# Performance work log

Measured on AMD Instinct MI355X. Metric: run time of the kernel, lower is better.

## Reference

```python
import jax, jax.numpy as jnp
import numpy as np

D_MODEL = 1024
NUM_HEADS = 16
HEAD_DIM = D_MODEL // NUM_HEADS


def setup_inputs() -> dict:
    key = jax.random.key(0)
    ks = jax.random.split(key, 10)
    B, SQ, SK = 2, 2048, 2048
    scale = 1.0 / np.sqrt(D_MODEL)
    inp = {
        "x1": jax.random.normal(ks[0], (B, SQ, D_MODEL), jnp.float32),
        "x2": jax.random.normal(ks[1], (B, SK, D_MODEL), jnp.float32),
        "Wq": jax.random.normal(ks[2], (D_MODEL, D_MODEL), jnp.float32) * scale,
        "bq": jnp.zeros((D_MODEL,), jnp.float32),
        "Wk": jax.random.normal(ks[3], (D_MODEL, D_MODEL), jnp.float32) * scale,
        "bk": jnp.zeros((D_MODEL,), jnp.float32),
        "Wv": jax.random.normal(ks[4], (D_MODEL, D_MODEL), jnp.float32) * scale,
        "bv": jnp.zeros((D_MODEL,), jnp.float32),
        "Wo": jax.random.normal(ks[5], (D_MODEL, D_MODEL), jnp.float32) * scale,
        "bo": jnp.zeros((D_MODEL,), jnp.float32),
    }
    return inp


def reference(x1, x2, Wq, bq, Wk, bk, Wv, bv, Wo, bo):
    B, SQ, _ = x1.shape
    SK = x2.shape[1]
    # projections, then split into heads: [B, H, S, Dh]
    def split_heads(t, S):
        return t.reshape(B, S, NUM_HEADS, HEAD_DIM).transpose(0, 2, 1, 3)
    Q = split_heads(x1 @ Wq + bq, SQ)
    K = split_heads(x2 @ Wk + bk, SK)
    V = split_heads(x2 @ Wv + bv, SK)
    # note: original scales by 1/head_dim**0.5
    scores = jnp.einsum("bhqd,bhkd->bhqk", Q, K) / jnp.sqrt(
        jnp.asarray(HEAD_DIM, Q.dtype))
    attn = jax.nn.softmax(scores, axis=-1)
    ctx = jnp.einsum("bhqk,bhkd->bhqd", attn, V)
    ctx = ctx.transpose(0, 2, 1, 3).reshape(B, SQ, D_MODEL)
    return ctx @ Wo + bo
```

## Files before the change

### kernel.cpp

```cpp
#include <hip/hip_runtime.h>
#include <stdint.h>


typedef unsigned short u16b;
typedef __attribute__((ext_vector_type(4))) short short4v;
typedef __attribute__((ext_vector_type(8))) short short8v;
typedef __attribute__((ext_vector_type(4))) float float4v;
typedef __attribute__((ext_vector_type(2))) unsigned int uint2v;

#if __has_builtin(__builtin_amdgcn_exp2f)
__device__ __forceinline__ float exp2_fast(float x){ return __builtin_amdgcn_exp2f(x); }
#else
__device__ __forceinline__ float exp2_fast(float x){ return exp2f(x); }
#endif

__device__ __forceinline__ u16b f2bf(float f) {
  union { float f; unsigned int i; } v; v.f = f;
  return (u16b)((v.i + 0x7fffu + ((v.i >> 16) & 1u)) >> 16);
}
__device__ __forceinline__ void gl_lds16(const u16b* g, u16b* l) {
  __builtin_amdgcn_global_load_lds(
      (const __attribute__((address_space(1))) void*)g,
      (__attribute__((address_space(3))) void*)l, 16, 0, 0);
}

#define FENCE_BARRIER() do { asm volatile("" ::: "memory"); \
  __builtin_amdgcn_s_barrier(); asm volatile("" ::: "memory"); } while(0)
#define LGKM0() do { asm volatile("s_waitcnt lgkmcnt(0)" ::: "memory"); \
  __builtin_amdgcn_sched_barrier(0); } while(0)
#define VMCNT(n) do { asm volatile("s_waitcnt vmcnt(" #n ")" ::: "memory"); \
  __builtin_amdgcn_sched_barrier(0); } while(0)

__global__ __launch_bounds__(256) void prep(
    const float* __restrict__ x1, const float* __restrict__ x2,
    const float* __restrict__ W0, const float* __restrict__ W1,
    const float* __restrict__ W2, const float* __restrict__ W3,
    u16b* __restrict__ x1b, u16b* __restrict__ x2b, u16b* __restrict__ WT) {
  const int tid = threadIdx.x;
  const int mode = blockIdx.y;
  if (mode < 2) {
    const float* src = mode ? x2 : x1;
    u16b* dst = mode ? x2b : x1b;
    const int n4 = 1024*1024;
    int i = blockIdx.x * 256 + tid;
    const int stride = gridDim.x * 256;
    for (; i < n4; i += stride) {
      float4v v = ((const float4v*)src)[i];
      short4v o;
      o[0]=(short)f2bf(v[0]); o[1]=(short)f2bf(v[1]);
      o[2]=(short)f2bf(v[2]); o[3]=(short)f2bf(v[3]);
      ((short4v*)dst)[i] = o;
    }
  } else {
    __shared__ u16b tile[32][33];
    const int z = mode - 2;
    const float* src = (z==0) ? W0 : (z==1) ? W1 : (z==2) ? W2 : W3;
    u16b* dst = WT + (size_t)z * (1024*1024);
    const int x = tid & 31, y = tid >> 5;
    const int bx = (blockIdx.x & 31) * 32, by = (blockIdx.x >> 5) * 32;
#pragma unroll
    for (int j=0;j<4;++j)
      tile[y*4+j][x] = f2bf(src[(size_t)(by + y*4+j)*1024 + bx + x]);
    __syncthreads();
#pragma unroll
    for (int j=0;j<4;++j)
      dst[(size_t)(bx + y*4+j)*1024 + by + x] = tile[x][y*4+j];
  }
}

template<bool BIAS_ROW>
__device__ __forceinline__ void gemm256_core(
    u16b* __restrict__ As, u16b* __restrict__ Bs,
    const u16b* __restrict__ A, const u16b* __restrict__ Bt,
    const float* __restrict__ bias, u16b* __restrict__ C,
    int N, int K, int bm, int bn, float oscale) {
  constexpr int ASTR = 256*64, BSTR = 256*64;
  const int tid = threadIdx.x;
  const int lane = tid & 63, wave = tid >> 6;
  const int wr = wave >> 2, wc = wave & 3;
  const int l15 = lane & 15, l4 = lane >> 4;

  auto stage_half = [&](const u16b* __restrict__ G, int row0, int k0,
                        u16b* __restrict__ Lbase) {
#pragma unroll
    for (int j=0;j<2;++j) {
      int idx = j*512 + tid;
      int row = idx >> 3, seg = idx & 7;
      int segg = seg ^ (row & 7);
      gl_lds16(&G[(size_t)(row0+row)*K + k0 + segg*8], &Lbase[idx*8]);
    }
  };

  float4v acc[2][2][4][2];
#pragma unroll
  for (int qm=0;qm<2;++qm)
#pragma unroll
  for (int qn=0;qn<2;++qn)
#pragma unroll
  for (int m=0;m<4;++m)
#pragma unroll
  for (int n=0;n<2;++n) acc[qm][qn][m][n] = (float4v){0.f,0.f,0.f,0.f};

  const int NK = K >> 6;
  stage_half(A,  bm+0,   0,  As + 0);
  stage_half(Bt, bn+0,   0,  Bs + 0);
  stage_half(A,  bm+128, 0,  As + 128*64);
  stage_half(Bt, bn+128, 0,  Bs + 128*64);
  stage_half(A,  bm+0,   64, As + ASTR);
  stage_half(Bt, bn+0,   64, Bs + BSTR);
  VMCNT(4);
  FENCE_BARRIER();

  int cur = 0;
  for (int t = 0; t < NK; ++t) {
    u16b* Ac = As + cur*ASTR;  u16b* Bc = Bs + cur*BSTR;
    u16b* An = As + (cur^1)*ASTR;  u16b* Bn = Bs + (cur^1)*BSTR;
    const int k1 = (t+1) << 6, k2 = (t+2) << 6;
    short8v af[4][2], bf0[2][2], bf1[2][2];

#pragma unroll
    for (int m=0;m<4;++m)
#pragma unroll
      for (int ks=0;ks<2;++ks)
        af[m][ks] = *(const short8v*)&Ac[(0*128 + wr*64 + m*16 + l15)*64
                                         + (((ks*4+l4) ^ (l15&7))*8)];
#pragma unroll
    for (int n=0;n<2;++n)
#pragma unroll
      for (int ks=0;ks<2;++ks)
        bf0[n][ks] = *(const short8v*)&Bc[(0*128 + wc*32 + n*16 + l15)*64
                                          + (((ks*4+l4) ^ (l15&7))*8)];
    if (t+1 < NK) stage_half(A, bm+128, k1, An + 128*64);
    FENCE_BARRIER();
    LGKM0();
    __builtin_amdgcn_s_setprio(1);
#pragma unroll
    for (int m=0;m<4;++m)
#pragma unroll
      for (int n=0;n<2;++n)
#pragma unroll
        for (int ks=0;ks<2;++ks)
          acc[0][0][m][n] = __builtin_amdgcn_mfma_f32_16x16x32_bf16(
              af[m][ks], bf0[n][ks], acc[0][0][m][n], 0, 0, 0);
    __builtin_amdgcn_s_setprio(0);
    FENCE_BARRIER();

#pragma unroll
    for (int n=0;n<2;++n)
#pragma unroll
      for (int ks=0;ks<2;++ks)
        bf1[n][ks] = *(const short8v*)&Bc[(1*128 + wc*32 + n*16 + l15)*64
                                          + (((ks*4+l4) ^ (l15&7))*8)];
    if (t+1 < NK) stage_half(Bt, bn+128, k1, Bn + 128*64);
    FENCE_BARRIER();
    LGKM0();
    __builtin_amdgcn_s_setprio(1);
#pragma unroll
    for (int m=0;m<4;++m)
#pragma unroll
      for (int n=0;n<2;++n)
#pragma unroll
        for (int ks=0;ks<2;++ks)
          acc[0][1][m][n] = __builtin_amdgcn_mfma_f32_16x16x32_bf16(
              af[m][ks], bf1[n][ks], acc[0][1][m][n], 0, 0, 0);
    __builtin_amdgcn_s_setprio(0);
    FENCE_BARRIER();

#pragma unroll
    for (int m=0;m<4;++m)
#pragma unroll
      for (int ks=0;ks<2;++ks)
        af[m][ks] = *(const short8v*)&Ac[(1*128 + wr*64 + m*16 + l15)*64
                                         + (((ks*4+l4) ^ (l15&7))*8)];
    if (t+2 < NK) stage_half(A, bm+0, k2, Ac + 0);
    FENCE_BARRIER();
    LGKM0();
    __builtin_amdgcn_s_setprio(1);
#pragma unroll
    for (int m=0;m<4;++m)
#pragma unroll
      for (int n=0;n<2;++n)
#pragma unroll
        for (int ks=0;ks<2;++ks)
          acc[1][0][m][n] = __builtin_amdgcn_mfma_f32_16x16x32_bf16(
              af[m][ks], bf0[n][ks], acc[1][0][m][n], 0, 0, 0);
    __builtin_amdgcn_s_setprio(0);
    FENCE_BARRIER();

    if (t+2 < NK) stage_half(Bt, bn+0, k2, Bc + 0);
    FENCE_BARRIER();
    LGKM0();
    __builtin_amdgcn_s_setprio(1);
#pragma unroll
    for (int m=0;m<4;++m)
#pragma unroll
      for (int n=0;n<2;++n)
#pragma unroll
        for (int ks=0;ks<2;++ks)
          acc[1][1][m][n] = __builtin_amdgcn_mfma_f32_16x16x32_bf16(
              af[m][ks], bf1[n][ks], acc[1][1][m][n], 0, 0, 0);
    __builtin_amdgcn_s_setprio(0);
    if (t == NK-2) { VMCNT(0); }
    else          { VMCNT(4); }
    FENCE_BARRIER();
    cur ^= 1;
  }

#pragma unroll
  for (int qm=0;qm<2;++qm)
#pragma unroll
  for (int qn=0;qn<2;++qn)
#pragma unroll
  for (int n=0;n<2;++n) {
    int col = bn + qn*128 + wc*32 + n*16 + l15;
    float bbc = BIAS_ROW ? 0.f : bias[col];
#pragma unroll
    for (int m=0;m<4;++m) {
      int row0 = bm + qm*128 + wr*64 + m*16 + l4*4;
#pragma unroll
      for (int r=0;r<4;++r) {
        float bb = BIAS_ROW ? bias[row0+r] : bbc;
        float v = (acc[qm][qn][m][n][r] + bb) * oscale;
        C[(size_t)(row0+r)*N + col] = f2bf(v);
      }
    }
  }
}

__global__ __launch_bounds__(512, 2) void gemm_qkv256(
    const u16b* __restrict__ x1b, const u16b* __restrict__ x2b,
    const u16b* __restrict__ WT, const float* __restrict__ bq,
    const float* __restrict__ bk, const float* __restrict__ bv,
    u16b* __restrict__ QKV) {
  __shared__ __align__(16) u16b As[2*256*64];
  __shared__ __align__(16) u16b Bs[2*256*64];
  const int f = blockIdx.x;
  const int z = f >> 6;
  const int u = f & 63;
  const int w = ((u & 7) << 3) | (u >> 3);
  const size_t Mi = 1024*1024;
  const float QSCALE = 0.125f * 1.4426950408889634f;
  if (z == 2) {
    int bm = (w >> 4) * 256;
    int bn = (w & 15) * 256;
    gemm256_core<true>(As, Bs, WT + 2*Mi, x2b, bv, QKV + 8*Mi,
                       4096, 1024, bm, bn, 1.0f);
  } else {
    int bm = (w >> 2) * 256;
    int bn = (w & 3) * 256;
    gemm256_core<false>(As, Bs, z ? x2b : x1b, WT + (size_t)z*Mi,
                        z ? bk : bq, QKV + (size_t)z*4*Mi,
                        1024, 1024, bm, bn, z ? 1.0f : QSCALE);
  }
}

template<int BN, bool OUT_F32, bool BIAS_ROW>
__device__ __forceinline__ void gemm_core(
    u16b* __restrict__ As, u16b* __restrict__ Bs,
    const u16b* __restrict__ A, const u16b* __restrict__ Bt,
    const float* __restrict__ bias, void* __restrict__ Cv,
    int N, int K, int bm, int bn, float oscale) {
  constexpr int NT = BN / 32;
  constexpr int ASTRIDE = 128*64;
  constexpr int BSTRIDE = BN*64;
  const int tid = threadIdx.x;
  const int lane = tid & 63, wave = tid >> 6;
  const int wm = wave >> 1, wn = wave & 1;
  const int l15 = lane & 15, l4 = lane >> 4;
  float4v acc[4][NT];
#pragma unroll
  for (int i=0;i<4;++i)
#pragma unroll
    for (int j=0;j<NT;++j) acc[i][j] = (float4v){0.f,0.f,0.f,0.f};

  auto stage = [&](int buf, int k0) {
#pragma unroll
    for (int j=0;j<4;++j) {
      int idx = j*256 + tid;
      int row = idx >> 3, seg = idx & 7;
      int segg = seg ^ (row & 7);
      gl_lds16(&A[(size_t)(bm+row)*K + k0 + segg*8], &As[buf*ASTRIDE + idx*8]);
    }
#pragma unroll
    for (int j=0;j<BN/32;++j) {
      int idx = j*256 + tid;
      int row = idx >> 3, seg = idx & 7;
      int segg = seg ^ (row & 7);
      gl_lds16(&Bt[(size_t)(bn+row)*K + k0 + segg*8], &Bs[buf*BSTRIDE + idx*8]);
    }
  };

  const int NK = K >> 6;
  stage(0, 0);
  __syncthreads();
  for (int kt = 0; kt < NK; ++kt) {
    const int cur = kt & 1;
    if (kt + 1 < NK) stage(cur ^ 1, (kt + 1) << 6);
    const u16b* Asb = As + cur*ASTRIDE;
    const u16b* Bsb = Bs + cur*BSTRIDE;
#pragma unroll
    for (int ks=0; ks<2; ++ks) {
      short8v af[4], bf[NT];
      const int cs = ((ks*4 + l4) ^ (l15 & 7)) * 8;
#pragma unroll
      for (int mt=0;mt<4;++mt)
        af[mt] = *(const short8v*)&Asb[(wm*64+mt*16+l15)*64 + cs];
#pragma unroll
      for (int nt=0;nt<NT;++nt)
        bf[nt] = *(const short8v*)&Bsb[(wn*(BN/2)+nt*16+l15)*64 + cs];
#pragma unroll
      for (int mt=0;mt<4;++mt)
#pragma unroll
        for (int nt=0;nt<NT;++nt)
          acc[mt][nt] = __builtin_amdgcn_mfma_f32_16x16x32_bf16(af[mt], bf[nt], acc[mt][nt], 0, 0, 0);
    }
    __syncthreads();
  }

#pragma unroll
  for (int nt=0;nt<NT;++nt) {
    int col = bn + wn*(BN/2) + nt*16 + l15;
    float bbc = BIAS_ROW ? 0.f : bias[col];
#pragma unroll
    for (int mt=0;mt<4;++mt) {
      int row0 = bm + wm*64 + mt*16 + l4*4;
#pragma unroll
      for (int r=0;r<4;++r) {
        float bb = BIAS_ROW ? bias[row0+r] : bbc;
        float v = (acc[mt][nt][r] + bb) * oscale;
        if (OUT_F32) ((float*)Cv)[(size_t)(row0+r)*N + col] = v;
        else         ((u16b*)Cv)[(size_t)(row0+r)*N + col] = f2bf(v);
      }
    }
  }
}

__global__ __launch_bounds__(256) void gemm_out(
    const u16b* __restrict__ A, const u16b* __restrict__ Bt,
    const float* __restrict__ bias, float* __restrict__ C) {
  __shared__ __align__(16) u16b As[2*128*64];
  __shared__ __align__(16) u16b Bs[2*64*64];
  const int f = blockIdx.x;
  const int xcd = f & 7, s = f >> 3;
  const int bm = (xcd*4 + (s >> 4)) * 128;
  const int bn = (s & 15) * 64;
  gemm_core<64,true,false>(As, Bs, A, Bt, bias, C, 1024, 1024, bm, bn, 1.0f);
}

__device__ __forceinline__ void attn_load(
    const u16b* __restrict__ Kgb, const u16b* __restrict__ Vtb,
    int kvoff, int tid, short8v kreg[4], short8v vreg[4]) {
#pragma unroll
  for (int j=0; j<4; ++j) {
    int idx = j*256 + tid;
    int rowk = idx >> 3, segk = idx & 7;
    kreg[j] = *(const short8v*)&Kgb[(size_t)(kvoff+rowk)*1024 + ((segk ^ (rowk & 7))*8)];
    int rowv = idx >> 4, segv = idx & 15;
    vreg[j] = *(const short8v*)&Vtb[(size_t)rowv*4096 + kvoff + ((segv ^ (rowv & 15))*8)];
  }
}

__global__ __launch_bounds__(256, 2) void attn_q128(
    const u16b* __restrict__ Q, const u16b* __restrict__ Kg,
    const u16b* __restrict__ Vt, u16b* __restrict__ O) {
  __shared__ __align__(16) u16b Ks[128*64];
  __shared__ __align__(16) u16b Vs[64*128];
  __shared__ __align__(16) u16b Ps[4*2*1024];
  const int tid = threadIdx.x;
  const int lane = tid & 63, wave = tid >> 6;
  const int l15 = lane & 15, l4 = lane >> 4;
  const int bh = blockIdx.x;
  const int b = bh >> 4, h = bh & 15;
  const int q0 = blockIdx.y * 128;
  const size_t seqbase = (size_t)b * 2048;
  const int colh = h * 64;
  const u16b* Kgb = Kg + seqbase*1024 + colh;
  const u16b* Vtb = Vt + (size_t)(h*64)*4096 + (size_t)b*2048;
  u16b* Pw = Ps + wave * 2048;

  short8v kreg[4], vreg[4];
  attn_load(Kgb, Vtb, 0, tid, kreg, vreg);

  short8v qf[2][2];
#pragma unroll
  for (int g=0; g<2; ++g) {
    size_t qrow = seqbase + q0 + wave*32 + g*16 + l15;
#pragma unroll
    for (int ks=0; ks<2; ++ks)
      qf[g][ks] = *(const short8v*)&Q[qrow*1024 + colh + ks*32 + l4*8];
  }

  short8v ones;
#pragma unroll
  for (int i=0;i<8;++i) ones[i] = (short)0x3F80;

  float4v lacc[2] = {(float4v){0.f,0.f,0.f,0.f}, (float4v){0.f,0.f,0.f,0.f}};
  float4v oacc[2][4];
#pragma unroll
  for (int g=0; g<2; ++g)
#pragma unroll
    for (int nb=0; nb<4; ++nb) oacc[g][nb] = (float4v){0.f,0.f,0.f,0.f};

  for (int kt = 0; kt < 16; ++kt) {
    __syncthreads();
#pragma unroll
    for (int j=0; j<4; ++j) {
      int idx = j*256 + tid;
      *(short8v*)&Ks[idx*8] = kreg[j];
      *(short8v*)&Vs[idx*8] = vreg[j];
    }
    __syncthreads();
    if (kt < 15)
      attn_load(Kgb, Vtb, (kt+1)*128, tid, kreg, vreg);

    float4v sacc[2][8];
#pragma unroll
    for (int g=0; g<2; ++g)
#pragma unroll
      for (int nb=0; nb<8; ++nb) sacc[g][nb] = (float4v){0.f,0.f,0.f,0.f};
#pragma unroll
    for (int nb=0; nb<8; ++nb)
#pragma unroll
      for (int ks=0; ks<2; ++ks) {
        short8v kf = *(const short8v*)&Ks[(nb*16+l15)*64 + (((ks*4+l4) ^ (l15 & 7))*8)];
        sacc[0][nb] = __builtin_amdgcn_mfma_f32_16x16x32_bf16(kf, qf[0][ks], sacc[0][nb], 0, 0, 0);
        sacc[1][nb] = __builtin_amdgcn_mfma_f32_16x16x32_bf16(kf, qf[1][ks], sacc[1][nb], 0, 0, 0);
      }

#pragma unroll
    for (int h2=0; h2<2; ++h2) {
#pragma unroll
      for (int g=0; g<2; ++g)
#pragma unroll
        for (int nbl=0; nbl<4; ++nbl) {
          const float4v s4 = sacc[g][h2*4 + nbl];
          unsigned int u0 = __float_as_uint(exp2_fast(s4[0]));
          unsigned int u1 = __float_as_uint(exp2_fast(s4[1]));
          unsigned int u2 = __float_as_uint(exp2_fast(s4[2]));
          unsigned int u3 = __float_as_uint(exp2_fast(s4[3]));
          uint2v dw;
          dw[0] = (u0 >> 16) | (u1 & 0xFFFF0000u);
          dw[1] = (u2 >> 16) | (u3 & 0xFFFF0000u);
          *(uint2v*)&Pw[g*1024 + l15*64 + (((nbl*4 + l4) ^ l15)*4)] = dw;
        }
      asm volatile("s_waitcnt lgkmcnt(0)" ::: "memory");

#pragma unroll
      for (int ks2=0; ks2<2; ++ks2) {
        short8v pf[2];
#pragma unroll
        for (int g=0; g<2; ++g) {
          int c0 = (ks2*8 + l4*2) ^ l15;
          int c1 = (ks2*8 + l4*2 + 1) ^ l15;
          short4v pa = *(const short4v*)&Pw[g*1024 + l15*64 + c0*4];
          short4v pb = *(const short4v*)&Pw[g*1024 + l15*64 + c1*4];
          short8v p;
          p[0]=pa[0]; p[1]=pa[1]; p[2]=pa[2]; p[3]=pa[3];
          p[4]=pb[0]; p[5]=pb[1]; p[6]=pb[2]; p[7]=pb[3];
          pf[g] = p;
          lacc[g] = __builtin_amdgcn_mfma_f32_16x16x32_bf16(p, ones, lacc[g], 0, 0, 0);
        }
#pragma unroll
        for (int nb=0; nb<4; ++nb) {
          int cc = (h2*8 + ks2*4 + l4) ^ l15;
          short8v vf = *(const short8v*)&Vs[(nb*16+l15)*128 + cc*8];
          oacc[0][nb] = __builtin_amdgcn_mfma_f32_16x16x32_bf16(pf[0], vf, oacc[0][nb], 0, 0, 0);
          oacc[1][nb] = __builtin_amdgcn_mfma_f32_16x16x32_bf16(pf[1], vf, oacc[1][nb], 0, 0, 0);
        }
      }
    }
  }

#pragma unroll
  for (int g=0; g<2; ++g)
#pragma unroll
    for (int r=0; r<4; ++r) {
      float inv = 1.0f / lacc[g][r];
      size_t row = seqbase + q0 + wave*32 + g*16 + l4*4 + r;
#pragma unroll
      for (int nb=0; nb<4; ++nb)
        O[row*1024 + colh + nb*16 + l15] = f2bf(oacc[g][nb][r] * inv);
    }
}

extern "C" void kernel_launch(void* const* d_in, const int* in_sizes, int n_in,
                              void* d_out, int out_size, void* d_ws, size_t ws_size,
                              hipStream_t stream) {
  const float* x1 = (const float*)d_in[0];
  const float* x2 = (const float*)d_in[1];
  const float* Wq = (const float*)d_in[2];
  const float* bq = (const float*)d_in[3];
  const float* Wk = (const float*)d_in[4];
  const float* bk = (const float*)d_in[5];
  const float* Wv = (const float*)d_in[6];
  const float* bv = (const float*)d_in[7];
  const float* Wo = (const float*)d_in[8];
  const float* bo = (const float*)d_in[9];
  (void)in_sizes; (void)n_in; (void)out_size; (void)ws_size;

  u16b* ws = (u16b*)d_ws;
  const size_t Mi = 1024*1024;
  u16b* WT  = ws;
  u16b* WoT = ws + 3*Mi;
  u16b* x1b = ws + 4*Mi;
  u16b* x2b = ws + 8*Mi;
  u16b* QKV = ws + 12*Mi;
  u16b* Qb  = QKV;
  u16b* Kb  = QKV + 4*Mi;
  u16b* Vtb = QKV + 8*Mi;
  u16b* Cx  = x1b;

  prep<<<dim3(1024,6), 256, 0, stream>>>(x1, x2, Wq, Wk, Wv, Wo, x1b, x2b, WT);

  gemm_qkv256<<<dim3(192), 512, 0, stream>>>(x1b, x2b, WT, bq, bk, bv, QKV);

  attn_q128<<<dim3(32,16), 256, 0, stream>>>(Qb, Kb, Vtb, Cx);

  gemm_out<<<dim3(512), 256, 0, stream>>>(Cx, WoT, bo, (float*)d_out);
}
```

Measured before the change: 200.6 us.

## Keep attention probabilities in registers using 32x32 MFMA, drop LDS P staging

Restructures the attention inner loop to use 32x32x16 MFMA for S = K·Q^T, so the score accumulator layout matches the A-operand layout of 32x32x8 MFMA for P·V. Probabilities are exponentiated, packed to bf16 with a byte-perm and fed straight into the PV MFMA without round-tripping through LDS. The row sum is now accumulated with scalar adds plus a cross-lane shuffle instead of an extra MFMA against a ones vector, and s_setprio is raised around the MFMA bursts. This removes the LDS writes, waits and reads for P and the extra MFMAs, at the cost of different register pressure and fragment layouts.

```diff
diff --git a/kernel.cpp b/kernel.cpp
--- a/kernel.cpp
+++ b/kernel.cpp
@@ -6,6 +6,7 @@
 typedef __attribute__((ext_vector_type(4))) short short4v;
 typedef __attribute__((ext_vector_type(8))) short short8v;
 typedef __attribute__((ext_vector_type(4))) float float4v;
+typedef __attribute__((ext_vector_type(16))) float float16v;
 typedef __attribute__((ext_vector_type(2))) unsigned int uint2v;
 
 #if __has_builtin(__builtin_amdgcn_exp2f)
@@ -365,10 +366,9 @@
     const u16b* __restrict__ Vt, u16b* __restrict__ O) {
   __shared__ __align__(16) u16b Ks[128*64];
   __shared__ __align__(16) u16b Vs[64*128];
-  __shared__ __align__(16) u16b Ps[4*2*1024];
   const int tid = threadIdx.x;
   const int lane = tid & 63, wave = tid >> 6;
-  const int l15 = lane & 15, l4 = lane >> 4;
+  const int l31 = lane & 31, hi = lane >> 5;
   const int bh = blockIdx.x;
   const int b = bh >> 4, h = bh & 15;
   const int q0 = blockIdx.y * 128;
@@ -376,30 +376,24 @@
   const int colh = h * 64;
   const u16b* Kgb = Kg + seqbase*1024 + colh;
   const u16b* Vtb = Vt + (size_t)(h*64)*4096 + (size_t)b*2048;
-  u16b* Pw = Ps + wave * 2048;
 
   short8v kreg[4], vreg[4];
   attn_load(Kgb, Vtb, 0, tid, kreg, vreg);
 
-  short8v qf[2][2];
-#pragma unroll
-  for (int g=0; g<2; ++g) {
-    size_t qrow = seqbase + q0 + wave*32 + g*16 + l15;
-#pragma unroll
-    for (int ks=0; ks<2; ++ks)
-      qf[g][ks] = *(const short8v*)&Q[qrow*1024 + colh + ks*32 + l4*8];
-  }
-
-  short8v ones;
-#pragma unroll
-  for (int i=0;i<8;++i) ones[i] = (short)0x3F80;
-
-  float4v lacc[2] = {(float4v){0.f,0.f,0.f,0.f}, (float4v){0.f,0.f,0.f,0.f}};
-  float4v oacc[2][4];
-#pragma unroll
-  for (int g=0; g<2; ++g)
-#pragma unroll
-    for (int nb=0; nb<4; ++nb) oacc[g][nb] = (float4v){0.f,0.f,0.f,0.f};
+  short8v qf[4];
+  {
+    size_t qrow = seqbase + q0 + wave*32 + l31;
+#pragma unroll
+    for (int ks=0; ks<4; ++ks)
+      qf[ks] = *(const short8v*)&Q[qrow*1024 + colh + ks*16 + hi*8];
+  }
+
+  float16v oacc[2];
+#pragma unroll
+  for (int nb=0; nb<2; ++nb)
+#pragma unroll
+    for (int r=0; r<16; ++r) oacc[nb][r] = 0.f;
+  float lsum = 0.f;
 
   for (int kt = 0; kt < 16; ++kt) {
     __syncthreads();
@@ -413,74 +407,61 @@
     if (kt < 15)
       attn_load(Kgb, Vtb, (kt+1)*128, tid, kreg, vreg);
 
-    float4v sacc[2][8];
-#pragma unroll
-    for (int g=0; g<2; ++g)
-#pragma unroll
-      for (int nb=0; nb<8; ++nb) sacc[g][nb] = (float4v){0.f,0.f,0.f,0.f};
-#pragma unroll
-    for (int nb=0; nb<8; ++nb)
-#pragma unroll
-      for (int ks=0; ks<2; ++ks) {
-        short8v kf = *(const short8v*)&Ks[(nb*16+l15)*64 + (((ks*4+l4) ^ (l15 & 7))*8)];
-        sacc[0][nb] = __builtin_amdgcn_mfma_f32_16x16x32_bf16(kf, qf[0][ks], sacc[0][nb], 0, 0, 0);
-        sacc[1][nb] = __builtin_amdgcn_mfma_f32_16x16x32_bf16(kf, qf[1][ks], sacc[1][nb], 0, 0, 0);
+    float16v sacc[4];
+#pragma unroll
+    for (int kb=0; kb<4; ++kb)
+#pragma unroll
+      for (int r=0; r<16; ++r) sacc[kb][r] = 0.f;
+    __builtin_amdgcn_s_setprio(1);
+#pragma unroll
+    for (int kb=0; kb<4; ++kb)
+#pragma unroll
+      for (int ks=0; ks<4; ++ks) {
+        int row = kb*32 + l31;
+        short8v kf = *(const short8v*)&Ks[row*64 + (((ks*2+hi) ^ (row & 7))*8)];
+        sacc[kb] = __builtin_amdgcn_mfma_f32_32x32x16_bf16(kf, qf[ks], sacc[kb], 0, 0, 0);
       }
-
-#pragma unroll
-    for (int h2=0; h2<2; ++h2) {
-#pragma unroll
-      for (int g=0; g<2; ++g)
-#pragma unroll
-        for (int nbl=0; nbl<4; ++nbl) {
-          const float4v s4 = sacc[g][h2*4 + nbl];
-          unsigned int u0 = __float_as_uint(exp2_fast(s4[0]));
-          unsigned int u1 = __float_as_uint(exp2_fast(s4[1]));
-          unsigned int u2 = __float_as_uint(exp2_fast(s4[2]));
-          unsigned int u3 = __float_as_uint(exp2_fast(s4[3]));
-          uint2v dw;
-          dw[0] = (u0 >> 16) | (u1 & 0xFFFF0000u);
-          dw[1] = (u2 >> 16) | (u3 & 0xFFFF0000u);
-          *(uint2v*)&Pw[g*1024 + l15*64 + (((nbl*4 + l4) ^ l15)*4)] = dw;
-        }
-      asm volatile("s_waitcnt lgkmcnt(0)" ::: "memory");
-
-#pragma unroll
-      for (int ks2=0; ks2<2; ++ks2) {
-        short8v pf[2];
-#pragma unroll
-        for (int g=0; g<2; ++g) {
-          int c0 = (ks2*8 + l4*2) ^ l15;
-          int c1 = (ks2*8 + l4*2 + 1) ^ l15;
-          short4v pa = *(const short4v*)&Pw[g*1024 + l15*64 + c0*4];
-          short4v pb = *(const short4v*)&Pw[g*1024 + l15*64 + c1*4];
-          short8v p;
-          p[0]=pa[0]; p[1]=pa[1]; p[2]=pa[2]; p[3]=pa[3];
-          p[4]=pb[0]; p[5]=pb[1]; p[6]=pb[2]; p[7]=pb[3];
-          pf[g] = p;
-          lacc[g] = __builtin_amdgcn_mfma_f32_16x16x32_bf16(p, ones, lacc[g], 0, 0, 0);
-        }
-#pragma unroll
-        for (int nb=0; nb<4; ++nb) {
-          int cc = (h2*8 + ks2*4 + l4) ^ l15;
-          short8v vf = *(const short8v*)&Vs[(nb*16+l15)*128 + cc*8];
-          oacc[0][nb] = __builtin_amdgcn_mfma_f32_16x16x32_bf16(pf[0], vf, oacc[0][nb], 0, 0, 0);
-          oacc[1][nb] = __builtin_amdgcn_mfma_f32_16x16x32_bf16(pf[1], vf, oacc[1][nb], 0, 0, 0);
+    __builtin_amdgcn_s_setprio(0);
+
+#pragma unroll
+    for (int kb=0; kb<4; ++kb) {
+      float e[16];
+#pragma unroll
+      for (int r=0; r<16; ++r) e[r] = exp2_fast(sacc[kb][r]);
+#pragma unroll
+      for (int r=0; r<16; ++r) lsum += e[r];
+      unsigned int d[8];
+#pragma unroll
+      for (int i=0; i<8; ++i)
+        d[i] = __builtin_amdgcn_perm(__float_as_uint(e[2*i+1]),
+                                     __float_as_uint(e[2*i]), 0x07060302u);
+      __builtin_amdgcn_s_setprio(1);
+#pragma unroll
+      for (int s=0; s<4; ++s) {
+        union { unsigned int u[2]; short4v s4; } pu;
+        pu.u[0] = d[2*s]; pu.u[1] = d[2*s+1];
+        const short4v pf = pu.s4;
+#pragma unroll
+        for (int nb=0; nb<2; ++nb) {
+          int row = nb*32 + l31;
+          short4v vf = *(const short4v*)&Vs[row*128 + (((kb*4+s) ^ (row & 15))*8) + hi*4];
+          oacc[nb] = __builtin_amdgcn_mfma_f32_32x32x8bf16_1k(pf, vf, oacc[nb], 0, 0, 0);
         }
       }
-    }
-  }
-
-#pragma unroll
-  for (int g=0; g<2; ++g)
-#pragma unroll
-    for (int r=0; r<4; ++r) {
-      float inv = 1.0f / lacc[g][r];
-      size_t row = seqbase + q0 + wave*32 + g*16 + l4*4 + r;
-#pragma unroll
-      for (int nb=0; nb<4; ++nb)
-        O[row*1024 + colh + nb*16 + l15] = f2bf(oacc[g][nb][r] * inv);
-    }
+      __builtin_amdgcn_s_setprio(0);
+    }
+  }
+
+  float ltot = lsum + __shfl_xor(lsum, 32, 64);
+#pragma unroll
+  for (int r=0; r<16; ++r) {
+    int qloc = (r & 3) + 8*(r >> 2) + 4*hi;
+    float lv = __shfl(ltot, qloc, 64);
+    float inv = 1.0f / lv;
+    size_t row = seqbase + q0 + wave*32 + qloc;
+    O[row*1024 + colh +      l31] = f2bf(oacc[0][r] * inv);
+    O[row*1024 + colh + 32 + l31] = f2bf(oacc[1][r] * inv);
+  }
 }
 
 extern "C" void kernel_launch(void* const* d_in, const int* in_sizes, int n_in,
```

New measurement: 204.7 us. 2.0% more time.
